# Performance work log

Hardware: AMD Instinct MI355X
Metric: run time of the kernel (lower is better)

Reference implementation:

```python
import jax, jax.numpy as jnp
import numpy as np

SIZE = 48          # sinkhorn_canvas_size
EPS = 0.01         # entropy regularization
ITERS = 5          # sinkhorn iterations
CHANNEL = 0        # fixed channel (original picks a random one of 3)


def _build_cost_matrix(size):
    y, x = jnp.meshgrid(jnp.arange(size), jnp.arange(size), indexing='ij')
    pixels = jnp.stack((y.flatten(), x.flatten()), axis=1).astype(jnp.float32) / size  # [N,2]
    diff = pixels[:, None, :] - pixels[None, :, :]  # [N,N,2]
    return jnp.sum(diff * diff, axis=-1)            # [N,N]


def setup_inputs() -> dict:
    key = jax.random.key(0)
    k1, k2 = jax.random.split(key)
    B = 32
    img_pred = jax.random.uniform(k1, (B, 3, SIZE, SIZE), dtype=jnp.float32)
    img_target = jax.random.uniform(k2, (B, 3, SIZE, SIZE), dtype=jnp.float32)
    cost_matrix = _build_cost_matrix(SIZE)
    return {"img_pred": img_pred, "img_target": img_target, "cost_matrix": cost_matrix}


def reference(img_pred, img_target, cost_matrix):
    B = img_pred.shape[0]
    # fixed channel, flatten spatial dims -> [B, N]
    p = img_pred[:, CHANNEL].reshape(B, -1) + 1e-9
    t = img_target[:, CHANNEL].reshape(B, -1) + 1e-9
    mass_source = p / jnp.sum(p, axis=-1, keepdims=True)
    mass_target = t / jnp.sum(t, axis=-1, keepdims=True)
    log_u = jnp.log(mass_source)
    log_v = jnp.log(mass_target)
    u = jnp.zeros_like(mass_source)
    v = jnp.zeros_like(mass_target)

    def M(u, v):
        # modified cost for log-domain updates: [B, N, N]
        return (-cost_matrix[None, :, :] + u[:, :, None] + v[:, None, :]) / EPS

    def lse(A):
        # matches torch: log(sum(exp(A), axis=2) + 1e-6)
        return jnp.log(jnp.sum(jnp.exp(A), axis=2) + 1e-6)

    for _ in range(ITERS):
        u = EPS * (log_u - lse(M(u, v))) + u
        v = EPS * (log_v - lse(jnp.swapaxes(M(u, v), 1, 2))) + v

    P = jnp.exp(M(u, v))                               # [B, N, N]
    cost = jnp.sum(P * cost_matrix[None, :, :], axis=(1, 2))  # [B]
    return cost
```

## Files before the change

kernel.cpp:

```cpp
#include <hip/hip_runtime.h>


#define SZ 48
#define SN 2304
#define LD 49
#define NBAT 32
#define NTHR 768
#define NW 12
#define YB 4

__global__ __launch_bounds__(256) void k_pre(const float* __restrict__ C,
                                             float* __restrict__ G,
                                             float* __restrict__ H) {
    const int idx = blockIdx.x * 256 + threadIdx.x;
    const int a = idx / SZ;
    const int c = idx - a * SZ;
    const float cv = C[(size_t)a * SZ * SN + (size_t)c * SZ];
    const float g = expf(-100.f * cv);
    G[idx] = g;
    H[idx] = g * cv;
}

__global__ __launch_bounds__(NTHR) void k_sink(const float* __restrict__ pred,
                                               const float* __restrict__ tgt,
                                               const float* __restrict__ Gm,
                                               const float* __restrict__ Hm,
                                               float* __restrict__ out) {
    __shared__ float Fa[SZ * LD];
    __shared__ float Fb[SZ * LD];
    __shared__ float Fms[SZ * LD];
    __shared__ float Fmt[SZ * LD];
    __shared__ float T[SZ * LD];
    __shared__ float gsl[SZ];
    __shared__ float red[32];

    const int t = threadIdx.x;
    const int b = blockIdx.x;
    const int l = t & 63;
    const int w = __builtin_amdgcn_readfirstlane(t >> 6);
    const int r0 = w * YB;

    if (t < SZ) {
        float s = 0.f;
        #pragma unroll 8
        for (int j = 0; j < SZ; ++j) s += Gm[t * SZ + j];
        gsl[t] = s;
    }
    const float* __restrict__ pg = pred + (size_t)b * 3 * SN;
    const float* __restrict__ tg = tgt + (size_t)b * 3 * SN;
    float sp = 0.f, st = 0.f;
    for (int i = t; i < SN; i += NTHR) {
        const float vp = pg[i] + 1e-9f;
        const float vt = tg[i] + 1e-9f;
        const int y = i / SZ, x = i - y * SZ;
        Fms[y * LD + x] = vp;
        Fmt[y * LD + x] = vt;
        sp += vp; st += vt;
    }
    #pragma unroll
    for (int off = 32; off; off >>= 1) {
        sp += __shfl_down(sp, off);
        st += __shfl_down(st, off);
    }
    if (l == 0) { red[w] = sp; red[16 + w] = st; }
    __syncthreads();
    float ps = 0.f, ts = 0.f;
    #pragma unroll
    for (int k = 0; k < NW; ++k) { ps += red[k]; ts += red[16 + k]; }
    for (int i = t; i < SN; i += NTHR) {
        const int y = i / SZ, x = i - y * SZ;
        const float ms = Fms[y * LD + x] / ps;
        Fms[y * LD + x] = ms;
        Fmt[y * LD + x] /= ts;
        Fa[y * LD + x] = ms / (gsl[y] * gsl[x] + 1e-6f);
        Fb[y * LD + x] = 1.f;
    }
    __syncthreads();

    for (int p = 1; p < 10; ++p) {
        float* __restrict__ src = (p & 1) ? Fa : Fb;
        float* __restrict__ dst = (p & 1) ? Fb : Fa;
        const float* __restrict__ mv = (p & 1) ? Fmt : Fms;

        if (l < SZ) {
            float acc[YB];
            #pragma unroll
            for (int k = 0; k < YB; ++k) acc[k] = 0.f;
            #pragma unroll 8
            for (int j = 0; j < SZ; ++j) {
                const float v = src[l * LD + j];
                #pragma unroll
                for (int k = 0; k < YB; ++k)
                    acc[k] = fmaf(Gm[j * SZ + r0 + k], v, acc[k]);
            }
            #pragma unroll
            for (int k = 0; k < YB; ++k) T[l * LD + r0 + k] = acc[k];
        }
        __syncthreads();

        if (l < SZ) {
            float acc[YB];
            #pragma unroll
            for (int k = 0; k < YB; ++k) acc[k] = 0.f;
            #pragma unroll 8
            for (int j = 0; j < SZ; ++j) {
                const float v = T[j * LD + l];
                #pragma unroll
                for (int k = 0; k < YB; ++k)
                    acc[k] = fmaf(Gm[j * SZ + r0 + k], v, acc[k]);
            }
            #pragma unroll
            for (int k = 0; k < YB; ++k) {
                const int idx = (r0 + k) * LD + l;
                const float yo = dst[idx];
                dst[idx] = mv[idx] * yo / (yo * acc[k] + 1e-6f);
            }
        }
        __syncthreads();
    }

    if (l < SZ) {
        float t1[YB], t2[YB];
        #pragma unroll
        for (int k = 0; k < YB; ++k) { t1[k] = 0.f; t2[k] = 0.f; }
        #pragma unroll 4
        for (int j = 0; j < SZ; ++j) {
            const float v = Fb[l * LD + j];
            #pragma unroll
            for (int k = 0; k < YB; ++k) {
                t1[k] = fmaf(Gm[j * SZ + r0 + k], v, t1[k]);
                t2[k] = fmaf(Hm[j * SZ + r0 + k], v, t2[k]);
            }
        }
        #pragma unroll
        for (int k = 0; k < YB; ++k) {
            T[l * LD + r0 + k]   = t1[k];
            Fms[l * LD + r0 + k] = t2[k];
        }
    }
    __syncthreads();

    float part = 0.f;
    if (l < SZ) {
        float u[YB];
        #pragma unroll
        for (int k = 0; k < YB; ++k) u[k] = 0.f;
        #pragma unroll 4
        for (int j = 0; j < SZ; ++j) {
            const float v1 = T[j * LD + l];
            const float v2 = Fms[j * LD + l];
            #pragma unroll
            for (int k = 0; k < YB; ++k) {
                u[k] = fmaf(Hm[j * SZ + r0 + k], v1, u[k]);
                u[k] = fmaf(Gm[j * SZ + r0 + k], v2, u[k]);
            }
        }
        #pragma unroll
        for (int k = 0; k < YB; ++k)
            part = fmaf(Fa[(r0 + k) * LD + l], u[k], part);
    }
    #pragma unroll
    for (int off = 32; off; off >>= 1) part += __shfl_down(part, off);
    if (l == 0) red[w] = part;
    __syncthreads();
    if (t == 0) {
        float c = 0.f;
        #pragma unroll
        for (int k = 0; k < NW; ++k) c += red[k];
        out[b] = c;
    }
}

extern "C" void kernel_launch(void* const* d_in, const int* in_sizes, int n_in,
                              void* d_out, int out_size, void* d_ws, size_t ws_size,
                              hipStream_t stream) {
    const float* pred = (const float*)d_in[0];
    const float* tgt  = (const float*)d_in[1];
    const float* C    = (const float*)d_in[2];
    float* G = (float*)d_ws;
    float* H = G + SN;

    k_pre<<<9, 256, 0, stream>>>(C, G, H);
    k_sink<<<NBAT, NTHR, 0, stream>>>(pred, tgt, G, H, (float*)d_out);
}
```

Measured before the change: 101.9 us.

## Vectorize separable Sinkhorn convolutions with float4 LDS loads and packed FMA

Pads the shared-memory row stride from 49 to 52 so each row is 16-byte aligned and can be read with float4 loads. The intermediate T is stored transposed, so both convolution passes read contiguous rows. Each thread also loads its four G/H kernel coefficients as one float4 and accumulates into float2 vectors, so the compiler can emit packed FMA instructions. The cost is LDS bank conflicts from the stride of 52 and from the transposed stores, plus higher register use from full unrolling.

```diff
diff --git a/kernel.cpp b/kernel.cpp
--- a/kernel.cpp
+++ b/kernel.cpp
@@ -3,11 +3,21 @@
 
 #define SZ 48
 #define SN 2304
-#define LD 49
+#define LD 52
 #define NBAT 32
 #define NTHR 768
 #define NW 12
 #define YB 4
+
+typedef float f2 __attribute__((ext_vector_type(2)));
+
+__device__ __forceinline__ f2 pkfma(f2 a, f2 b, f2 c) {
+#if __has_builtin(__builtin_elementwise_fma)
+    return __builtin_elementwise_fma(a, b, c);
+#else
+    f2 r; r.x = fmaf(a.x, b.x, c.x); r.y = fmaf(a.y, b.y, c.y); return r;
+#endif
+}
 
 __global__ __launch_bounds__(256) void k_pre(const float* __restrict__ C,
                                              float* __restrict__ G,
@@ -21,6 +31,24 @@
     H[idx] = g * cv;
 }
 
+#define CONV_STEP(row, Mm, a0, a1)                                          \
+    {                                                                       \
+        _Pragma("unroll")                                                   \
+        for (int jc = 0; jc < 12; ++jc) {                                   \
+            const float4 q = *(const float4*)&(row)[jc * 4];                \
+            _Pragma("unroll")                                               \
+            for (int jj = 0; jj < 4; ++jj) {                                \
+                const int j = jc * 4 + jj;                                  \
+                const float4 g = *(const float4*)((Mm) + j * SZ + r0);      \
+                const float v = (jj == 0) ? q.x : (jj == 1) ? q.y           \
+                              : (jj == 2) ? q.z : q.w;                      \
+                const f2 vv = {v, v};                                       \
+                a0 = pkfma((f2){g.x, g.y}, vv, a0);                         \
+                a1 = pkfma((f2){g.z, g.w}, vv, a1);                         \
+            }                                                               \
+        }                                                                   \
+    }
+
 __global__ __launch_bounds__(NTHR) void k_sink(const float* __restrict__ pred,
                                                const float* __restrict__ tgt,
                                                const float* __restrict__ Gm,
@@ -30,7 +58,7 @@
     __shared__ float Fb[SZ * LD];
     __shared__ float Fms[SZ * LD];
     __shared__ float Fmt[SZ * LD];
-    __shared__ float T[SZ * LD];
+    __shared__ float Tt[SZ * LD];
     __shared__ float gsl[SZ];
     __shared__ float red[32];
 
@@ -83,81 +111,84 @@
         const float* __restrict__ mv = (p & 1) ? Fmt : Fms;
 
         if (l < SZ) {
-            float acc[YB];
-            #pragma unroll
-            for (int k = 0; k < YB; ++k) acc[k] = 0.f;
-            #pragma unroll 8
-            for (int j = 0; j < SZ; ++j) {
-                const float v = src[l * LD + j];
-                #pragma unroll
-                for (int k = 0; k < YB; ++k)
-                    acc[k] = fmaf(Gm[j * SZ + r0 + k], v, acc[k]);
-            }
-            #pragma unroll
-            for (int k = 0; k < YB; ++k) T[l * LD + r0 + k] = acc[k];
+            f2 a0 = {0.f, 0.f}, a1 = {0.f, 0.f};
+            CONV_STEP(&src[l * LD], Gm, a0, a1);
+            Tt[(r0 + 0) * LD + l] = a0.x;
+            Tt[(r0 + 1) * LD + l] = a0.y;
+            Tt[(r0 + 2) * LD + l] = a1.x;
+            Tt[(r0 + 3) * LD + l] = a1.y;
         }
         __syncthreads();
 
         if (l < SZ) {
-            float acc[YB];
-            #pragma unroll
-            for (int k = 0; k < YB; ++k) acc[k] = 0.f;
-            #pragma unroll 8
-            for (int j = 0; j < SZ; ++j) {
-                const float v = T[j * LD + l];
-                #pragma unroll
-                for (int k = 0; k < YB; ++k)
-                    acc[k] = fmaf(Gm[j * SZ + r0 + k], v, acc[k]);
-            }
+            f2 a0 = {0.f, 0.f}, a1 = {0.f, 0.f};
+            CONV_STEP(&Tt[l * LD], Gm, a0, a1);
+            const float s4[4] = {a0.x, a0.y, a1.x, a1.y};
             #pragma unroll
             for (int k = 0; k < YB; ++k) {
                 const int idx = (r0 + k) * LD + l;
                 const float yo = dst[idx];
-                dst[idx] = mv[idx] * yo / (yo * acc[k] + 1e-6f);
+                dst[idx] = mv[idx] * yo / (yo * s4[k] + 1e-6f);
             }
         }
         __syncthreads();
     }
 
     if (l < SZ) {
-        float t1[YB], t2[YB];
-        #pragma unroll
-        for (int k = 0; k < YB; ++k) { t1[k] = 0.f; t2[k] = 0.f; }
-        #pragma unroll 4
-        for (int j = 0; j < SZ; ++j) {
-            const float v = Fb[l * LD + j];
+        f2 t1a = {0.f, 0.f}, t1b = {0.f, 0.f};
+        f2 t2a = {0.f, 0.f}, t2b = {0.f, 0.f};
+        #pragma unroll
+        for (int jc = 0; jc < 12; ++jc) {
+            const float4 q = *(const float4*)&Fb[l * LD + jc * 4];
             #pragma unroll
-            for (int k = 0; k < YB; ++k) {
-                t1[k] = fmaf(Gm[j * SZ + r0 + k], v, t1[k]);
-                t2[k] = fmaf(Hm[j * SZ + r0 + k], v, t2[k]);
+            for (int jj = 0; jj < 4; ++jj) {
+                const int j = jc * 4 + jj;
+                const float4 g = *(const float4*)(Gm + j * SZ + r0);
+                const float4 h = *(const float4*)(Hm + j * SZ + r0);
+                const float v = (jj == 0) ? q.x : (jj == 1) ? q.y
+                              : (jj == 2) ? q.z : q.w;
+                const f2 vv = {v, v};
+                t1a = pkfma((f2){g.x, g.y}, vv, t1a);
+                t1b = pkfma((f2){g.z, g.w}, vv, t1b);
+                t2a = pkfma((f2){h.x, h.y}, vv, t2a);
+                t2b = pkfma((f2){h.z, h.w}, vv, t2b);
             }
         }
-        #pragma unroll
-        for (int k = 0; k < YB; ++k) {
-            T[l * LD + r0 + k]   = t1[k];
-            Fms[l * LD + r0 + k] = t2[k];
-        }
+        Tt [(r0 + 0) * LD + l] = t1a.x;  Tt [(r0 + 1) * LD + l] = t1a.y;
+        Tt [(r0 + 2) * LD + l] = t1b.x;  Tt [(r0 + 3) * LD + l] = t1b.y;
+        Fms[(r0 + 0) * LD + l] = t2a.x;  Fms[(r0 + 1) * LD + l] = t2a.y;
+        Fms[(r0 + 2) * LD + l] = t2b.x;  Fms[(r0 + 3) * LD + l] = t2b.y;
     }
     __syncthreads();
 
     float part = 0.f;
     if (l < SZ) {
-        float u[YB];
-        #pragma unroll
-        for (int k = 0; k < YB; ++k) u[k] = 0.f;
-        #pragma unroll 4
-        for (int j = 0; j < SZ; ++j) {
-            const float v1 = T[j * LD + l];
-            const float v2 = Fms[j * LD + l];
+        f2 u0 = {0.f, 0.f}, u1 = {0.f, 0.f};
+        #pragma unroll
+        for (int jc = 0; jc < 12; ++jc) {
+            const float4 q1 = *(const float4*)&Tt [l * LD + jc * 4];
+            const float4 q2 = *(const float4*)&Fms[l * LD + jc * 4];
             #pragma unroll
-            for (int k = 0; k < YB; ++k) {
-                u[k] = fmaf(Hm[j * SZ + r0 + k], v1, u[k]);
-                u[k] = fmaf(Gm[j * SZ + r0 + k], v2, u[k]);
+            for (int jj = 0; jj < 4; ++jj) {
+                const int j = jc * 4 + jj;
+                const float4 g = *(const float4*)(Gm + j * SZ + r0);
+                const float4 h = *(const float4*)(Hm + j * SZ + r0);
+                const float v1 = (jj == 0) ? q1.x : (jj == 1) ? q1.y
+                               : (jj == 2) ? q1.z : q1.w;
+                const float v2 = (jj == 0) ? q2.x : (jj == 1) ? q2.y
+                               : (jj == 2) ? q2.z : q2.w;
+                const f2 vv1 = {v1, v1};
+                const f2 vv2 = {v2, v2};
+                u0 = pkfma((f2){h.x, h.y}, vv1, u0);
+                u1 = pkfma((f2){h.z, h.w}, vv1, u1);
+                u0 = pkfma((f2){g.x, g.y}, vv2, u0);
+                u1 = pkfma((f2){g.z, g.w}, vv2, u1);
             }
         }
+        const float u4[4] = {u0.x, u0.y, u1.x, u1.y};
         #pragma unroll
         for (int k = 0; k < YB; ++k)
-            part = fmaf(Fa[(r0 + k) * LD + l], u[k], part);
+            part = fmaf(Fa[(r0 + k) * LD + l], u4[k], part);
     }
     #pragma unroll
     for (int off = 32; off; off >>= 1) part += __shfl_down(part, off);
```

Measured after the change: 104.9 us. 2.9% more time.

## Pack Gaussian kernel per wave as float4, widen block, vectorize LDS row reads

Applied to the files above, without the earlier changes.

Repacks the separable Gaussian factor G and G*C into per-wave float4 groups of three columns (padded), so each wave reads its three rows with one vector load per j. The block grows from 12 to 16 waves, each handling 3 rows instead of 4. The shared-memory row stride becomes 52 so each thread can read its full 48-float row into registers with float4 LDS loads. The intermediate T is now stored transposed so the second pass also reads rows. This adds register pressure and 25% padding waste in the G loads.

```diff
diff --git a/kernel.cpp b/kernel.cpp
--- a/kernel.cpp
+++ b/kernel.cpp
@@ -3,34 +3,38 @@
 
 #define SZ 48
 #define SN 2304
-#define LD 49
+#define LD 52
 #define NBAT 32
-#define NTHR 768
-#define NW 12
-#define YB 4
+#define NTHR 1024
+#define NW 16
+#define YB 3
 
 __global__ __launch_bounds__(256) void k_pre(const float* __restrict__ C,
-                                             float* __restrict__ G,
-                                             float* __restrict__ H) {
+                                             float* __restrict__ Gp,
+                                             float* __restrict__ Hp) {
     const int idx = blockIdx.x * 256 + threadIdx.x;
-    const int a = idx / SZ;
-    const int c = idx - a * SZ;
-    const float cv = C[(size_t)a * SZ * SN + (size_t)c * SZ];
-    const float g = expf(-100.f * cv);
-    G[idx] = g;
-    H[idx] = g * cv;
+    const int j   = idx / SZ;
+    const int col = idx - j * SZ;
+    const int w   = col / 3;
+    const int c   = col - w * 3;
+    const float cv = C[(size_t)j * SZ * SN + (size_t)col * SZ];
+    const float g  = expf(-100.f * cv);
+    const int base = (w * SZ + j) * 4;
+    Gp[base + c] = g;
+    Hp[base + c] = g * cv;
+    if (c == 0) { Gp[base + 3] = 0.f; Hp[base + 3] = 0.f; }
 }
 
 __global__ __launch_bounds__(NTHR) void k_sink(const float* __restrict__ pred,
                                                const float* __restrict__ tgt,
-                                               const float* __restrict__ Gm,
-                                               const float* __restrict__ Hm,
+                                               const float* __restrict__ Gpg,
+                                               const float* __restrict__ Hpg,
                                                float* __restrict__ out) {
     __shared__ float Fa[SZ * LD];
     __shared__ float Fb[SZ * LD];
     __shared__ float Fms[SZ * LD];
     __shared__ float Fmt[SZ * LD];
-    __shared__ float T[SZ * LD];
+    __shared__ float Tt[SZ * LD];
     __shared__ float gsl[SZ];
     __shared__ float red[32];
 
@@ -40,10 +44,15 @@
     const int w = __builtin_amdgcn_readfirstlane(t >> 6);
     const int r0 = w * YB;
 
+    const float4* __restrict__ Gp4 = (const float4*)Gpg + (size_t)w * SZ;
+    const float4* __restrict__ Hp4 = (const float4*)Hpg + (size_t)w * SZ;
+
     if (t < SZ) {
+        const int wc = t / 3, cc = t - wc * 3;
         float s = 0.f;
         #pragma unroll 8
-        for (int j = 0; j < SZ; ++j) s += Gm[t * SZ + j];
+        for (int j = 0; j < SZ; ++j)
+            s += Gpg[(wc * SZ + j) * 4 + cc];
         gsl[t] = s;
     }
     const float* __restrict__ pg = pred + (size_t)b * 3 * SN;
@@ -83,77 +92,107 @@
         const float* __restrict__ mv = (p & 1) ? Fmt : Fms;
 
         if (l < SZ) {
-            float acc[YB];
-            #pragma unroll
-            for (int k = 0; k < YB; ++k) acc[k] = 0.f;
-            #pragma unroll 8
+            float4 q[12];
+            #pragma unroll
+            for (int jc = 0; jc < 12; ++jc)
+                q[jc] = *(const float4*)&src[l * LD + jc * 4];
+            float a0 = 0.f, a1 = 0.f, a2 = 0.f;
+            #pragma unroll
             for (int j = 0; j < SZ; ++j) {
-                const float v = src[l * LD + j];
-                #pragma unroll
-                for (int k = 0; k < YB; ++k)
-                    acc[k] = fmaf(Gm[j * SZ + r0 + k], v, acc[k]);
+                const float4 g = Gp4[j];
+                const float v = (j & 3) == 0 ? q[j >> 2].x
+                              : (j & 3) == 1 ? q[j >> 2].y
+                              : (j & 3) == 2 ? q[j >> 2].z : q[j >> 2].w;
+                a0 = fmaf(g.x, v, a0);
+                a1 = fmaf(g.y, v, a1);
+                a2 = fmaf(g.z, v, a2);
             }
-            #pragma unroll
-            for (int k = 0; k < YB; ++k) T[l * LD + r0 + k] = acc[k];
+            Tt[(r0 + 0) * LD + l] = a0;
+            Tt[(r0 + 1) * LD + l] = a1;
+            Tt[(r0 + 2) * LD + l] = a2;
         }
         __syncthreads();
 
         if (l < SZ) {
-            float acc[YB];
-            #pragma unroll
-            for (int k = 0; k < YB; ++k) acc[k] = 0.f;
-            #pragma unroll 8
+            float4 q[12];
+            #pragma unroll
+            for (int jc = 0; jc < 12; ++jc)
+                q[jc] = *(const float4*)&Tt[l * LD + jc * 4];
+            float a0 = 0.f, a1 = 0.f, a2 = 0.f;
+            #pragma unroll
             for (int j = 0; j < SZ; ++j) {
-                const float v = T[j * LD + l];
-                #pragma unroll
-                for (int k = 0; k < YB; ++k)
-                    acc[k] = fmaf(Gm[j * SZ + r0 + k], v, acc[k]);
+                const float4 g = Gp4[j];
+                const float v = (j & 3) == 0 ? q[j >> 2].x
+                              : (j & 3) == 1 ? q[j >> 2].y
+                              : (j & 3) == 2 ? q[j >> 2].z : q[j >> 2].w;
+                a0 = fmaf(g.x, v, a0);
+                a1 = fmaf(g.y, v, a1);
+                a2 = fmaf(g.z, v, a2);
             }
+            const float s3[3] = {a0, a1, a2};
             #pragma unroll
             for (int k = 0; k < YB; ++k) {
                 const int idx = (r0 + k) * LD + l;
                 const float yo = dst[idx];
-                dst[idx] = mv[idx] * yo / (yo * acc[k] + 1e-6f);
+                dst[idx] = mv[idx] * yo / (yo * s3[k] + 1e-6f);
             }
         }
         __syncthreads();
     }
 
     if (l < SZ) {
-        float t1[YB], t2[YB];
-        #pragma unroll
-        for (int k = 0; k < YB; ++k) { t1[k] = 0.f; t2[k] = 0.f; }
-        #pragma unroll 4
+        float4 q[12];
+        #pragma unroll
+        for (int jc = 0; jc < 12; ++jc)
+            q[jc] = *(const float4*)&Fb[l * LD + jc * 4];
+        float t1[3] = {0.f, 0.f, 0.f}, t2[3] = {0.f, 0.f, 0.f};
+        #pragma unroll
         for (int j = 0; j < SZ; ++j) {
-            const float v = Fb[l * LD + j];
-            #pragma unroll
-            for (int k = 0; k < YB; ++k) {
-                t1[k] = fmaf(Gm[j * SZ + r0 + k], v, t1[k]);
-                t2[k] = fmaf(Hm[j * SZ + r0 + k], v, t2[k]);
-            }
+            const float4 g = Gp4[j];
+            const float4 h = Hp4[j];
+            const float v = (j & 3) == 0 ? q[j >> 2].x
+                          : (j & 3) == 1 ? q[j >> 2].y
+                          : (j & 3) == 2 ? q[j >> 2].z : q[j >> 2].w;
+            t1[0] = fmaf(g.x, v, t1[0]);
+            t1[1] = fmaf(g.y, v, t1[1]);
+            t1[2] = fmaf(g.z, v, t1[2]);
+            t2[0] = fmaf(h.x, v, t2[0]);
+            t2[1] = fmaf(h.y, v, t2[1]);
+            t2[2] = fmaf(h.z, v, t2[2]);
         }
         #pragma unroll
         for (int k = 0; k < YB; ++k) {
-            T[l * LD + r0 + k]   = t1[k];
-            Fms[l * LD + r0 + k] = t2[k];
+            Tt [(r0 + k) * LD + l] = t1[k];
+            Fms[(r0 + k) * LD + l] = t2[k];
         }
     }
     __syncthreads();
 
     float part = 0.f;
     if (l < SZ) {
-        float u[YB];
-        #pragma unroll
-        for (int k = 0; k < YB; ++k) u[k] = 0.f;
-        #pragma unroll 4
+        float4 q1[12], q2[12];
+        #pragma unroll
+        for (int jc = 0; jc < 12; ++jc) {
+            q1[jc] = *(const float4*)&Tt [l * LD + jc * 4];
+            q2[jc] = *(const float4*)&Fms[l * LD + jc * 4];
+        }
+        float u[3] = {0.f, 0.f, 0.f};
+        #pragma unroll
         for (int j = 0; j < SZ; ++j) {
-            const float v1 = T[j * LD + l];
-            const float v2 = Fms[j * LD + l];
-            #pragma unroll
-            for (int k = 0; k < YB; ++k) {
-                u[k] = fmaf(Hm[j * SZ + r0 + k], v1, u[k]);
-                u[k] = fmaf(Gm[j * SZ + r0 + k], v2, u[k]);
-            }
+            const float4 g = Gp4[j];
+            const float4 h = Hp4[j];
+            const float v1 = (j & 3) == 0 ? q1[j >> 2].x
+                           : (j & 3) == 1 ? q1[j >> 2].y
+                           : (j & 3) == 2 ? q1[j >> 2].z : q1[j >> 2].w;
+            const float v2 = (j & 3) == 0 ? q2[j >> 2].x
+                           : (j & 3) == 1 ? q2[j >> 2].y
+                           : (j & 3) == 2 ? q2[j >> 2].z : q2[j >> 2].w;
+            u[0] = fmaf(h.x, v1, u[0]);
+            u[1] = fmaf(h.y, v1, u[1]);
+            u[2] = fmaf(h.z, v1, u[2]);
+            u[0] = fmaf(g.x, v2, u[0]);
+            u[1] = fmaf(g.y, v2, u[1]);
+            u[2] = fmaf(g.z, v2, u[2]);
         }
         #pragma unroll
         for (int k = 0; k < YB; ++k)
@@ -177,9 +216,9 @@
     const float* pred = (const float*)d_in[0];
     const float* tgt  = (const float*)d_in[1];
     const float* C    = (const float*)d_in[2];
-    float* G = (float*)d_ws;
-    float* H = G + SN;
-
-    k_pre<<<9, 256, 0, stream>>>(C, G, H);
-    k_sink<<<NBAT, NTHR, 0, stream>>>(pred, tgt, G, H, (float*)d_out);
+    float* Gp = (float*)d_ws;
+    float* Hp = Gp + NW * SZ * 4;
+
+    k_pre<<<9, 256, 0, stream>>>(C, Gp, Hp);
+    k_sink<<<NBAT, NTHR, 0, stream>>>(pred, tgt, Gp, Hp, (float*)d_out);
 }
```

After: 110.7 us. 1.09x slower.

## Transpose intermediate tile, use float4 LDS row reads, and widen block to 16 waves

Applied to the files above, without the earlier changes.

Stores the first-pass separable convolution result transposed so that both passes read contiguous rows from shared memory with float4 loads. The row pitch is padded from 49 to 52 so those loads stay 16-byte aligned. Threads per block rise from 768 to 1024 (16 waves, 3 rows each instead of 12 waves with 4 rows each), which spreads the per-batch work across more waves. The aim is fewer LDS instructions and more latency hiding, at the cost of possible bank conflicts on the strided transposed writes and more register pressure under the larger launch bound.

```diff
diff --git a/kernel.cpp b/kernel.cpp
--- a/kernel.cpp
+++ b/kernel.cpp
@@ -3,11 +3,11 @@
 
 #define SZ 48
 #define SN 2304
-#define LD 49
+#define LD 52
 #define NBAT 32
-#define NTHR 768
-#define NW 12
-#define YB 4
+#define NTHR 1024
+#define NW 16
+#define YB 3
 
 __global__ __launch_bounds__(256) void k_pre(const float* __restrict__ C,
                                              float* __restrict__ G,
@@ -21,6 +21,10 @@
     H[idx] = g * cv;
 }
 
+__device__ __forceinline__ float getc(const float4 v, int i) {
+    return i == 0 ? v.x : i == 1 ? v.y : i == 2 ? v.z : v.w;
+}
+
 __global__ __launch_bounds__(NTHR) void k_sink(const float* __restrict__ pred,
                                                const float* __restrict__ tgt,
                                                const float* __restrict__ Gm,
@@ -30,7 +34,7 @@
     __shared__ float Fb[SZ * LD];
     __shared__ float Fms[SZ * LD];
     __shared__ float Fmt[SZ * LD];
-    __shared__ float T[SZ * LD];
+    __shared__ float Tt[SZ * LD];
     __shared__ float gsl[SZ];
     __shared__ float red[32];
 
@@ -83,76 +87,97 @@
         const float* __restrict__ mv = (p & 1) ? Fmt : Fms;
 
         if (l < SZ) {
-            float acc[YB];
-            #pragma unroll
-            for (int k = 0; k < YB; ++k) acc[k] = 0.f;
-            #pragma unroll 8
-            for (int j = 0; j < SZ; ++j) {
-                const float v = src[l * LD + j];
-                #pragma unroll
-                for (int k = 0; k < YB; ++k)
-                    acc[k] = fmaf(Gm[j * SZ + r0 + k], v, acc[k]);
-            }
-            #pragma unroll
-            for (int k = 0; k < YB; ++k) T[l * LD + r0 + k] = acc[k];
+            float a0 = 0.f, a1 = 0.f, a2 = 0.f;
+            #pragma unroll
+            for (int jc = 0; jc < 12; ++jc) {
+                const float4 q = *(const float4*)&src[l * LD + jc * 4];
+                #pragma unroll
+                for (int jj = 0; jj < 4; ++jj) {
+                    const int j = jc * 4 + jj;
+                    const float g0 = Gm[j * SZ + r0];
+                    const float g1 = Gm[j * SZ + r0 + 1];
+                    const float g2 = Gm[j * SZ + r0 + 2];
+                    const float v = getc(q, jj);
+                    a0 = fmaf(g0, v, a0);
+                    a1 = fmaf(g1, v, a1);
+                    a2 = fmaf(g2, v, a2);
+                }
+            }
+            Tt[(r0 + 0) * LD + l] = a0;
+            Tt[(r0 + 1) * LD + l] = a1;
+            Tt[(r0 + 2) * LD + l] = a2;
         }
         __syncthreads();
 
         if (l < SZ) {
-            float acc[YB];
-            #pragma unroll
-            for (int k = 0; k < YB; ++k) acc[k] = 0.f;
-            #pragma unroll 8
-            for (int j = 0; j < SZ; ++j) {
-                const float v = T[j * LD + l];
-                #pragma unroll
-                for (int k = 0; k < YB; ++k)
-                    acc[k] = fmaf(Gm[j * SZ + r0 + k], v, acc[k]);
-            }
+            float a0 = 0.f, a1 = 0.f, a2 = 0.f;
+            #pragma unroll
+            for (int jc = 0; jc < 12; ++jc) {
+                const float4 q = *(const float4*)&Tt[l * LD + jc * 4];
+                #pragma unroll
+                for (int jj = 0; jj < 4; ++jj) {
+                    const int j = jc * 4 + jj;
+                    const float g0 = Gm[j * SZ + r0];
+                    const float g1 = Gm[j * SZ + r0 + 1];
+                    const float g2 = Gm[j * SZ + r0 + 2];
+                    const float v = getc(q, jj);
+                    a0 = fmaf(g0, v, a0);
+                    a1 = fmaf(g1, v, a1);
+                    a2 = fmaf(g2, v, a2);
+                }
+            }
+            const float s3[3] = {a0, a1, a2};
             #pragma unroll
             for (int k = 0; k < YB; ++k) {
                 const int idx = (r0 + k) * LD + l;
                 const float yo = dst[idx];
-                dst[idx] = mv[idx] * yo / (yo * acc[k] + 1e-6f);
+                dst[idx] = mv[idx] * yo / (yo * s3[k] + 1e-6f);
             }
         }
         __syncthreads();
     }
 
     if (l < SZ) {
-        float t1[YB], t2[YB];
-        #pragma unroll
-        for (int k = 0; k < YB; ++k) { t1[k] = 0.f; t2[k] = 0.f; }
-        #pragma unroll 4
-        for (int j = 0; j < SZ; ++j) {
-            const float v = Fb[l * LD + j];
-            #pragma unroll
-            for (int k = 0; k < YB; ++k) {
-                t1[k] = fmaf(Gm[j * SZ + r0 + k], v, t1[k]);
-                t2[k] = fmaf(Hm[j * SZ + r0 + k], v, t2[k]);
+        float t1[3] = {0.f, 0.f, 0.f}, t2[3] = {0.f, 0.f, 0.f};
+        #pragma unroll
+        for (int jc = 0; jc < 12; ++jc) {
+            const float4 q = *(const float4*)&Fb[l * LD + jc * 4];
+            #pragma unroll
+            for (int jj = 0; jj < 4; ++jj) {
+                const int j = jc * 4 + jj;
+                const float v = getc(q, jj);
+                #pragma unroll
+                for (int k = 0; k < YB; ++k) {
+                    t1[k] = fmaf(Gm[j * SZ + r0 + k], v, t1[k]);
+                    t2[k] = fmaf(Hm[j * SZ + r0 + k], v, t2[k]);
+                }
             }
         }
         #pragma unroll
         for (int k = 0; k < YB; ++k) {
-            T[l * LD + r0 + k]   = t1[k];
-            Fms[l * LD + r0 + k] = t2[k];
+            Tt [(r0 + k) * LD + l] = t1[k];
+            Fms[(r0 + k) * LD + l] = t2[k];
         }
     }
     __syncthreads();
 
     float part = 0.f;
     if (l < SZ) {
-        float u[YB];
-        #pragma unroll
-        for (int k = 0; k < YB; ++k) u[k] = 0.f;
-        #pragma unroll 4
-        for (int j = 0; j < SZ; ++j) {
-            const float v1 = T[j * LD + l];
-            const float v2 = Fms[j * LD + l];
-            #pragma unroll
-            for (int k = 0; k < YB; ++k) {
-                u[k] = fmaf(Hm[j * SZ + r0 + k], v1, u[k]);
-                u[k] = fmaf(Gm[j * SZ + r0 + k], v2, u[k]);
+        float u[3] = {0.f, 0.f, 0.f};
+        #pragma unroll
+        for (int jc = 0; jc < 12; ++jc) {
+            const float4 q1 = *(const float4*)&Tt [l * LD + jc * 4];
+            const float4 q2 = *(const float4*)&Fms[l * LD + jc * 4];
+            #pragma unroll
+            for (int jj = 0; jj < 4; ++jj) {
+                const int j = jc * 4 + jj;
+                const float v1 = getc(q1, jj);
+                const float v2 = getc(q2, jj);
+                #pragma unroll
+                for (int k = 0; k < YB; ++k) {
+                    u[k] = fmaf(Hm[j * SZ + r0 + k], v1, u[k]);
+                    u[k] = fmaf(Gm[j * SZ + r0 + k], v2, u[k]);
+                }
             }
         }
         #pragma unroll
```

Result: slower. 115.7 us (+13.6%).
